# Optimization experiments

Measured on AMD Instinct MI355X. Metric: run time of the kernel, lower is better.

Reference implementation:

```python
import jax, jax.numpy as jnp
import numpy as np

MD = 4  # max_displacement
NEG_SLOPE = 0.1

def _lrelu(x):
    return jnp.where(x >= 0, x, NEG_SLOPE * x)

def _conv3x3(x, w, b):
    # x: [B,C,H,W], w: [O,I,3,3]
    y = jax.lax.conv_general_dilated(x, w, (1, 1), 'SAME',
                                     dimension_numbers=('NCHW', 'OIHW', 'NCHW'))
    return y + b[None, :, None, None]

def _correlation(x_ref, x_nb, md=MD):
    # FlowNet-style correlation, kernel_size=1, stride1=stride2=1, pad=md.
    # out[:, dy*(2md+1)+dx, h, w] = mean_c x_ref[:,c,h,w] * x_nb_pad[:,c,h+dy,w+dx]
    B, C, H, W = x_ref.shape
    xp = jnp.pad(x_nb, ((0, 0), (0, 0), (md, md), (md, md)))
    outs = []
    for dy in range(2 * md + 1):
        for dx in range(2 * md + 1):
            sh = jax.lax.dynamic_slice(xp, (0, 0, dy, dx), (B, C, H, W))
            outs.append(jnp.einsum('bchw,bchw->bhw', x_ref, sh))
    return jnp.stack(outs, axis=1) / C  # [B, (2md+1)^2, H, W]

def _resize2x(x):
    # matches torch F.interpolate(scale_factor=2, mode='bilinear', align_corners=False)
    B, C, H, W = x.shape
    return jax.image.resize(x, (B, C, 2 * H, 2 * W), method='linear')

def setup_inputs() -> dict:
    key = jax.random.key(0)
    ks = jax.random.split(key, 12)
    B, C, H, W = 4, 32, 256, 256
    inner = 32
    corr_dim = (2 * MD + 1) ** 2  # 81
    cin = corr_dim + 32 + 2       # 115
    def wconv(k, o, i):
        return jax.random.normal(k, (o, i, 3, 3), jnp.float32) * 0.05
    return {
        'x_ref': jax.random.normal(ks[0], (B, C, H, W), jnp.float32),
        'x_neighbor': jax.random.normal(ks[1], (B, C, H, W), jnp.float32),
        'base_flow': jax.random.normal(ks[2], (B, 1, 2, H // 2, W // 2), jnp.float32),
        'base_feature': jax.random.normal(ks[3], (B, 32, H // 2, W // 2), jnp.float32),
        'w0': wconv(ks[4], inner, cin), 'b0': jnp.zeros((inner,), jnp.float32),
        'w1': wconv(ks[5], inner, inner), 'b1': jnp.zeros((inner,), jnp.float32),
        'w2': wconv(ks[6], inner, inner), 'b2': jnp.zeros((inner,), jnp.float32),
        'wf': wconv(ks[7], 3, inner), 'bf': jnp.zeros((3,), jnp.float32),
    }

def reference(x_ref, x_neighbor, base_flow, base_feature,
              w0, b0, w1, b1, w2, b2, wf, bf):
    corr = _lrelu(_correlation(x_ref, x_neighbor))           # [B,81,H,W]
    input_feats = _resize2x(base_feature)                    # [B,32,H,W]
    B, nf, two, h2, w2_ = base_flow.shape
    bflow = _resize2x(base_flow.reshape(B, nf * two, h2, w2_)) * 2.0  # [B,2,H,W]
    inp = jnp.concatenate([corr, input_feats, bflow], axis=1)  # [B,115,H,W]
    h = _lrelu(_conv3x3(inp, w0, b0))
    # BasicBlock
    t = _conv3x3(_lrelu(_conv3x3(h, w1, b1)), w2, b2) + h
    feats = _lrelu(t)                                        # [B,32,H,W]
    fm = _conv3x3(feats, wf, bf)                             # [B,3,H,W]
    flow_x, flow_y, mask = jnp.split(fm, 3, axis=1)
    flows = jnp.stack([flow_x, flow_y], axis=1)              # [B,2,1,H,W]
    mask = jax.nn.sigmoid(mask)
    return flows, mask, feats
```

## Files before the change

kernel.cpp:

```cpp
#include <hip/hip_runtime.h>

typedef unsigned short u16;
typedef unsigned int u32;
typedef __bf16 bf16x8 __attribute__((ext_vector_type(8)));
typedef float f32x4 __attribute__((ext_vector_type(4)));

#define HP 258
#define E_WT0 0
#define E_WT1 37120
#define E_WT2 46592
#define E_WTF 56064
#define C_CH      4260096ull
#define OFF_INPT  131072ull
#define S_INPT    17040384ull
#define OFF_HT    68292608ull
#define S_H       4260096ull
#define OFF_T1    85332992ull
#define OFF_FEA   102373376ull
#define OFF_XREFT 119413760ull
#define S_XREF    4194304ull
#define OFF_XNBT  136190976ull
#define S_XNB     4595712ull
#define WS_NEED   154573824ull
#define SE_INPT 8520192u
#define SE_H    2130048u
#define SE_XREF 2097152u
#define SE_XNB  2297856u

__device__ __forceinline__ float bf2f(u16 u){ u32 x = ((u32)u) << 16; return __builtin_bit_cast(float, x); }
__device__ __forceinline__ u16 f2bf(float f){
  u32 x = __builtin_bit_cast(u32, f);
  return (u16)((x + 0x7fffu + ((x >> 16) & 1u)) >> 16);
}
__device__ __forceinline__ u32 pack2(float a, float b){ return (u32)f2bf(a) | ((u32)f2bf(b) << 16); }
__device__ __forceinline__ float lrelu(float x){ return x >= 0.f ? x : 0.1f * x; }

__global__ void k_sent(float* __restrict__ out, float val){
  if (threadIdx.x == 0 && blockIdx.x == 0) out[0] = val;
}

__global__ __launch_bounds__(256) void k_halo(char* __restrict__ ws){
  int idx = blockIdx.x * 256 + threadIdx.x;
  const int bio = blockIdx.y;
  if (idx >= 258 * 258) return;
  int y = idx / 258;
  int x = idx - y * 258;
  if (y != 0 && y != 257 && x != 0 && x != 257) return;
  uint4 z = make_uint4(0u, 0u, 0u, 0u);
  size_t pix = (size_t)idx;
  #pragma unroll
  for (int s = 0; s < 4; s++){
    uint4* p0 = (uint4*)(ws + OFF_INPT + (size_t)bio * S_INPT + (size_t)s * C_CH + pix * 64);
    #pragma unroll
    for (int k = 0; k < 4; k++) p0[k] = z;
  }
  uint4* p1 = (uint4*)(ws + OFF_HT  + (size_t)bio * S_H + pix * 64);
  uint4* p2 = (uint4*)(ws + OFF_T1  + (size_t)bio * S_H + pix * 64);
  uint4* p3 = (uint4*)(ws + OFF_FEA + (size_t)bio * S_H + pix * 64);
  #pragma unroll
  for (int k = 0; k < 4; k++){ p1[k] = z; p2[k] = z; p3[k] = z; }
}

__global__ __launch_bounds__(256) void k_wprep(const float* __restrict__ w0, const float* __restrict__ w1,
    const float* __restrict__ w2, const float* __restrict__ wf, u16* __restrict__ wse){
  for (int idx = blockIdx.x * 256 + threadIdx.x; idx < 60800; idx += 64 * 256){
    float v = 0.f;
    if (idx < 37120){
      int co = idx / 1160, kk = idx % 1160;
      if (kk < 1152){
        int tap = kk >> 7, c = kk & 127;
        if (c < 115){
          int oc = (c < 34) ? (81 + c) : (c - 34);
          v = w0[(co * 115 + oc) * 9 + tap];
        }
      }
    } else if (idx < 46592){
      int r = idx - 37120; int co = r / 296, kk = r % 296;
      if (kk < 288){ int tap = kk >> 5, c = kk & 31; v = w1[(co * 32 + c) * 9 + tap]; }
    } else if (idx < 56064){
      int r = idx - 46592; int co = r / 296, kk = r % 296;
      if (kk < 288){ int tap = kk >> 5, c = kk & 31; v = w2[(co * 32 + c) * 9 + tap]; }
    } else {
      int r = idx - 56064; int co = r / 296, kk = r % 296;
      if (kk < 288 && co < 3){ int tap = kk >> 5, c = kk & 31; v = wf[(co * 32 + c) * 9 + tap]; }
    }
    wse[idx] = f2bf(v);
  }
}

__global__ __launch_bounds__(64) void k_xpose(const float* __restrict__ xref,
    const float* __restrict__ xnb, u16* __restrict__ xrefT0, u16* __restrict__ xnbT0){
  const int l = threadIdx.x;
  const int bxx = blockIdx.x;
  const int bio = blockIdx.y;
  const int cq = l & 3, c0 = cq * 8;
  float v[8];
  u32 p[4];
  if (bxx < 4096){
    const int row = bxx >> 4;
    const int px = ((bxx & 15) << 4) + (l >> 2);
    const float* src = xref + ((size_t)(bio * 32 + c0)) * 65536 + (size_t)row * 256 + px;
    #pragma unroll
    for (int k = 0; k < 8; k++) v[k] = src[(size_t)k * 65536];
    #pragma unroll
    for (int j = 0; j < 4; j++) p[j] = pack2(v[2 * j], v[2 * j + 1]);
    *(uint4*)(xrefT0 + (size_t)bio * SE_XREF + ((size_t)row * 256 + px) * 32 + c0) = *(uint4*)p;
  } else {
    const int i = bxx - 4096;
    const int hp = i / 17, pg = i - hp * 17;
    const int pt = pg * 16 + (l >> 2);
    const int ih = hp - 4, px = pt - 4;
    u16* dst = xnbT0 + (size_t)bio * SE_XNB + ((size_t)hp * 272 + pt) * 32 + c0;
    if (ih >= 0 && ih <= 255 && px >= 0 && px <= 255){
      const float* src = xnb + ((size_t)(bio * 32 + c0)) * 65536 + (size_t)ih * 256 + px;
      #pragma unroll
      for (int k = 0; k < 8; k++) v[k] = src[(size_t)k * 65536];
      #pragma unroll
      for (int j = 0; j < 4; j++) p[j] = pack2(v[2 * j], v[2 * j + 1]);
      *(uint4*)dst = *(uint4*)p;
    } else {
      uint4 z = make_uint4(0u, 0u, 0u, 0u);
      *(uint4*)dst = z;
    }
  }
}

__global__ __launch_bounds__(256) void k_up(const float* __restrict__ bflow,
    const float* __restrict__ bfeat, char* __restrict__ ws){
  const int w = threadIdx.x;
  const int bx = blockIdx.x;
  const int bio = blockIdx.y;
  const int h = (bx & 7) * 32 + (bx >> 3);
  int y0 = (h >> 1) - 1 + (h & 1);
  const float fy = (h & 1) ? 0.25f : 0.75f;
  const int y0o = (y0 < 0 ? 0 : y0) * 128;
  const int y1o = ((y0 + 1) > 127 ? 127 : (y0 + 1)) * 128;
  int x0 = (w >> 1) - 1 + (w & 1);
  const float fx = (w & 1) ? 0.25f : 0.75f;
  const int x0c = x0 < 0 ? 0 : x0;
  const int x1c = (x0 + 1) > 127 ? 127 : (x0 + 1);

  char* pxb = ws + OFF_INPT + (size_t)bio * S_INPT + ((size_t)(h + 1) * 258 + (w + 1)) * 64;

  u32 pk[16];
  #pragma unroll
  for (int d = 0; d < 16; d++){
    float vv[2];
    #pragma unroll
    for (int e = 0; e < 2; e++){
      const float* pl = bfeat + ((size_t)(bio * 32 + 2 * d + e)) * 16384;
      float v00 = pl[y0o + x0c], v01 = pl[y0o + x1c];
      float v10 = pl[y1o + x0c], v11 = pl[y1o + x1c];
      float r0 = v00 + fx * (v01 - v00);
      float r1 = v10 + fx * (v11 - v10);
      vv[e] = r0 + fy * (r1 - r0);
    }
    pk[d] = pack2(vv[0], vv[1]);
  }
  uint4* dst0 = (uint4*)pxb;
  #pragma unroll
  for (int q = 0; q < 4; q++) dst0[q] = ((uint4*)pk)[q];

  float fv[2];
  #pragma unroll
  for (int e = 0; e < 2; e++){
    const float* pl = bflow + ((size_t)(bio * 2 + e)) * 16384;
    float v00 = pl[y0o + x0c], v01 = pl[y0o + x1c];
    float v10 = pl[y1o + x0c], v11 = pl[y1o + x1c];
    float r0 = v00 + fx * (v01 - v00);
    float r1 = v10 + fx * (v11 - v10);
    fv[e] = (r0 + fy * (r1 - r0)) * 2.f;
  }
  *(u32*)(pxb + C_CH) = pack2(fv[0], fv[1]);

  *(u16*)(pxb + 3 * C_CH + 38) = 0;
  #pragma unroll
  for (int k2 = 0; k2 < 6; k2++) *(u32*)(pxb + 3 * C_CH + 40 + 4 * k2) = 0;
}

__global__ __launch_bounds__(256) void k_corr_mfma(const u16* __restrict__ xrefT0,
    const u16* __restrict__ xnbT0, char* __restrict__ ws){
  const int tid = threadIdx.x;
  const int wv = tid >> 6, l = tid & 63;
  const int bx = blockIdx.x;
  const int bio = blockIdx.y;
  const u16* xrefT = xrefT0 + (size_t)bio * SE_XREF;
  const u16* xnbT  = xnbT0  + (size_t)bio * SE_XNB;
  const int r = bx & 255, sub = bx >> 8;
  const int h = (r & 7) * 32 + (r >> 3);
  const int w0 = (sub * 4 + wv) * 16;
  const int m16 = l & 15, g = l >> 4;

  uint4 ua = *(const uint4*)(xrefT + ((size_t)h * 256 + w0 + m16) * 32 + g * 8);
  bf16x8 av = __builtin_bit_cast(bf16x8, ua);

  size_t bOff = ((size_t)h * 272 + w0 + m16) * 32 + g * 8;
  char* ob = ws + OFF_INPT + (size_t)bio * S_INPT
             + ((size_t)(h + 1) * 258 + (w0 + 1) + g * 4) * 64;
  const f32x4 z = {0.f, 0.f, 0.f, 0.f};
  #pragma unroll
  for (int dy = 0; dy < 9; dy++){
    uint4 ub0 = *(const uint4*)(xnbT + bOff);
    uint4 ub1 = *(const uint4*)(xnbT + bOff + 512);
    bOff += 8704;
    f32x4 d0 = __builtin_amdgcn_mfma_f32_16x16x32_bf16(av, __builtin_bit_cast(bf16x8, ub0), z, 0, 0, 0);
    f32x4 d1 = __builtin_amdgcn_mfma_f32_16x16x32_bf16(av, __builtin_bit_cast(bf16x8, ub1), z, 0, 0, 0);
    #pragma unroll
    for (int j = 0; j < 4; j++){
      int dxa = m16 - g * 4 - j;
      int dxb = dxa + 16;
      bool va = (unsigned)dxa <= 8u;
      bool vb = (unsigned)dxb <= 8u;
      if (va | vb){
        float val = va ? d0[j] : d1[j];
        int dx = va ? dxa : dxb;
        float f = lrelu(val * 0.03125f);
        int c = 34 + dy * 9 + dx;
        *(u16*)(ob + j * 64 + (size_t)(c >> 5) * C_CH + (c & 31) * 2) = f2bf(f);
      }
    }
  }
}

__global__ __launch_bounds__(256) void k_conv0(const u16* __restrict__ inT0, const u16* __restrict__ wt,
    const float* __restrict__ bias, u16* __restrict__ outA0){
  __shared__ __align__(16) u16 inL[12672];
  const int tid = threadIdx.x;
  const int bx = blockIdx.x;
  const int bio = blockIdx.y;
  const u16* inT = inT0 + (size_t)bio * SE_INPT;
  u16* outA = outA0 + (size_t)bio * SE_H;
  const int rq = (bx & 7) * 8 + ((bx >> 3) & 7);
  const int ph = bx >> 6;
  const int row0 = rq * 4, p0 = ph * 64;
  const int wv = tid >> 6, ln = tid & 63, l15 = ln & 15, l4 = ln >> 4;
  f32x4 acc[4][2] = {};

  for (int s = 0; s < 4; s++){
    for (int i = tid; i < 1584; i += 256){
      int rr = i / 264, q = i - rr * 264;
      int pxi = q >> 2, cq = q & 3;
      const u16* src = inT + ((size_t)s * 66564 + (size_t)(row0 + rr) * 258 + (p0 + pxi)) * 32 + cq * 8;
      ((uint4*)inL)[(rr * 66 + pxi) * 4 + cq] = *(const uint4*)src;
    }
    __syncthreads();
    #pragma unroll
    for (int ky = 0; ky < 3; ky++){
      #pragma unroll
      for (int kx = 0; kx < 3; kx++){
        const int tap = ky * 3 + kx;
        bf16x8 bv[2];
        #pragma unroll
        for (int j = 0; j < 2; j++){
          uint4 u = *(const uint4*)(wt + (size_t)(j * 16 + l15) * 1160 + tap * 128 + s * 32 + l4 * 8);
          bv[j] = __builtin_bit_cast(bf16x8, u);
        }
        #pragma unroll
        for (int t = 0; t < 4; t++){
          uint4 uai = *(const uint4*)&inL[((wv + ky) * 66 + t * 16 + l15 + kx) * 32 + l4 * 8];
          bf16x8 av = __builtin_bit_cast(bf16x8, uai);
          #pragma unroll
          for (int j = 0; j < 2; j++)
            acc[t][j] = __builtin_amdgcn_mfma_f32_16x16x32_bf16(av, bv[j], acc[t][j], 0, 0, 0);
        }
      }
    }
    __syncthreads();
  }
  const int row = row0 + wv;
  #pragma unroll
  for (int t = 0; t < 4; t++){
    const int pxb = p0 + t * 16 + l4 * 4;
    #pragma unroll
    for (int j = 0; j < 2; j++){
      const int co = j * 16 + l15;
      const float bs = bias[co];
      #pragma unroll
      for (int r = 0; r < 4; r++){
        const int px = pxb + r;
        float v = lrelu(acc[t][j][r] + bs);
        outA[(size_t)((row + 1) * HP + px + 1) * 32 + co] = f2bf(v);
      }
    }
  }
}

template<int NT, int MODE>
__global__ __launch_bounds__(256) void k_conv32(const u16* __restrict__ inT0, const u16* __restrict__ wt,
    const float* __restrict__ bias, u16* __restrict__ outH0, float* __restrict__ outF,
    const u16* __restrict__ resid0){
  __shared__ __align__(16) u16 inL[12672];
  const int tid = threadIdx.x;
  const int bx = blockIdx.x;
  const int bio = blockIdx.y;
  const u16* inT = inT0 + (size_t)bio * SE_H;
  const int rq = (bx & 7) * 8 + ((bx >> 3) & 7);
  const int ph = bx >> 6;
  const int row0 = rq * 4, p0 = ph * 64;
  const int wv = tid >> 6, ln = tid & 63, l15 = ln & 15, l4 = ln >> 4;

  for (int i = tid; i < 1584; i += 256){
    int rr = i / 264, q = i - rr * 264;
    int pxi = q >> 2, cq = q & 3;
    const u16* src = inT + ((size_t)(row0 + rr) * 258 + (p0 + pxi)) * 32 + cq * 8;
    ((uint4*)inL)[(rr * 66 + pxi) * 4 + cq] = *(const uint4*)src;
  }
  __syncthreads();

  f32x4 acc[4][NT] = {};
  #pragma unroll
  for (int ky = 0; ky < 3; ky++){
    #pragma unroll
    for (int kx = 0; kx < 3; kx++){
      const int tap = ky * 3 + kx;
      bf16x8 bv[NT];
      #pragma unroll
      for (int j = 0; j < NT; j++){
        uint4 u = *(const uint4*)(wt + (size_t)(j * 16 + l15) * 296 + tap * 32 + l4 * 8);
        bv[j] = __builtin_bit_cast(bf16x8, u);
      }
      #pragma unroll
      for (int t = 0; t < 4; t++){
        uint4 uai = *(const uint4*)&inL[((wv + ky) * 66 + t * 16 + l15 + kx) * 32 + l4 * 8];
        bf16x8 av = __builtin_bit_cast(bf16x8, uai);
        #pragma unroll
        for (int j = 0; j < NT; j++)
          acc[t][j] = __builtin_amdgcn_mfma_f32_16x16x32_bf16(av, bv[j], acc[t][j], 0, 0, 0);
      }
    }
  }
  const int row = row0 + wv;
  #pragma unroll
  for (int t = 0; t < 4; t++){
    const int pxb = p0 + t * 16 + l4 * 4;
    #pragma unroll
    for (int j = 0; j < NT; j++){
      const int co = j * 16 + l15;
      float bs;
      if constexpr (MODE == 2) bs = (co < 3) ? bias[co] : 0.f;
      else bs = bias[co];
      #pragma unroll
      for (int r = 0; r < 4; r++){
        const int px = pxb + r;
        float v = acc[t][j][r] + bs;
        if constexpr (MODE == 0){
          v = lrelu(v);
          outH0[(size_t)bio * SE_H + (size_t)((row + 1) * HP + px + 1) * 32 + co] = f2bf(v);
        } else if constexpr (MODE == 1){
          float hres = bf2f(resid0[(size_t)bio * SE_H + (size_t)((row + 1) * HP + px + 1) * 32 + co]);
          v = lrelu(v + hres);
          outH0[(size_t)bio * SE_H + (size_t)((row + 1) * HP + px + 1) * 32 + co] = f2bf(v);
          outF[786432 + ((size_t)(bio * 32 + co)) * 65536 + (size_t)row * 256 + px] = v;
        } else {
          if (co < 2)
            outF[((size_t)(bio * 2 + co)) * 65536 + (size_t)row * 256 + px] = v;
          else if (co == 2){
            float s = 1.f / (1.f + __expf(-v));
            outF[524288 + (size_t)bio * 65536 + (size_t)row * 256 + px] = s;
          }
        }
      }
    }
  }
}

extern "C" void kernel_launch(void* const* d_in, const int* in_sizes, int n_in,
                              void* d_out, int out_size, void* d_ws, size_t ws_size,
                              hipStream_t stream){
  float* out = (float*)d_out;

  static const int exp_sizes[12] = {8388608, 8388608, 131072, 2097152,
                                    33120, 32, 9216, 32, 9216, 32, 864, 3};
  float sent = 0.f;
  if (n_in != 12) sent = 1.0e6f;
  else if (out_size != 9175040) sent = 2.0e6f;
  else {
    for (int i = 0; i < 12; i++)
      if (in_sizes[i] != exp_sizes[i]){ sent = 3.0e6f * (1.0f + 0.01f * i); break; }
    if (sent == 0.f && ws_size < WS_NEED)
      sent = 16.0f * (float)(ws_size >> 20);
  }
  if (sent != 0.f){
    hipLaunchKernelGGL(k_sent, dim3(1), dim3(64), 0, stream, out, sent);
    return;
  }

  const float* xref  = (const float*)d_in[0];
  const float* xnb   = (const float*)d_in[1];
  const float* bflow = (const float*)d_in[2];
  const float* bfeat = (const float*)d_in[3];
  const float* w0 = (const float*)d_in[4];
  const float* b0 = (const float*)d_in[5];
  const float* w1 = (const float*)d_in[6];
  const float* b1 = (const float*)d_in[7];
  const float* w2 = (const float*)d_in[8];
  const float* b2 = (const float*)d_in[9];
  const float* wf = (const float*)d_in[10];
  const float* bf = (const float*)d_in[11];
  char* ws = (char*)d_ws;
  u16* wse   = (u16*)d_ws;
  u16* inpT  = (u16*)(ws + OFF_INPT);
  u16* hT    = (u16*)(ws + OFF_HT);
  u16* t1T   = (u16*)(ws + OFF_T1);
  u16* feaT  = (u16*)(ws + OFF_FEA);
  u16* xrefT = (u16*)(ws + OFF_XREFT);
  u16* xnbT  = (u16*)(ws + OFF_XNBT);

  hipLaunchKernelGGL(k_halo, dim3(261, 4), dim3(256), 0, stream, ws);
  hipLaunchKernelGGL(k_wprep, dim3(64), dim3(256), 0, stream, w0, w1, w2, wf, wse);
  hipLaunchKernelGGL(k_xpose, dim3(8584, 4), dim3(64), 0, stream, xref, xnb, xrefT, xnbT);
  hipLaunchKernelGGL(k_up, dim3(256, 4), dim3(256), 0, stream, bflow, bfeat, ws);
  hipLaunchKernelGGL(k_corr_mfma, dim3(1024, 4), dim3(256), 0, stream, xrefT, xnbT, ws);
  hipLaunchKernelGGL(k_conv0, dim3(256, 4), dim3(256), 0, stream, inpT, wse + E_WT0, b0, hT);
  hipLaunchKernelGGL((k_conv32<2, 0>), dim3(256, 4), dim3(256), 0, stream,
                     hT, wse + E_WT1, b1, t1T, (float*)nullptr, (const u16*)nullptr);
  hipLaunchKernelGGL((k_conv32<2, 1>), dim3(256, 4), dim3(256), 0, stream,
                     t1T, wse + E_WT2, b2, feaT, out, hT);
  hipLaunchKernelGGL((k_conv32<1, 2>), dim3(256, 4), dim3(256), 0, stream,
                     feaT, wse + E_WTF, bf, (u16*)nullptr, out, (const u16*)nullptr);
}
```

Measured before the change: 279.4 us.

## Merge prep kernels into one launch and XOR-swizzle conv LDS tiles

Four preprocessing kernels (halo zeroing, weight conversion, input transpose, upsample) are merged into a single k_prep launch that branches on block index, with the transpose using 256-thread blocks covering four waves each. This removes three launches and their gaps and lets the independent prep work run concurrently. The conv kernels also XOR-swizzle the channel-quad index in shared memory by pixel, to reduce LDS bank conflicts on the 16-byte MFMA operand reads. The merged kernel trades some branch divergence and less specialised blocks for fewer launches.

```diff
diff --git a/kernel.cpp b/kernel.cpp
--- a/kernel.cpp
+++ b/kernel.cpp
@@ -39,143 +39,141 @@
   if (threadIdx.x == 0 && blockIdx.x == 0) out[0] = val;
 }
 
-__global__ __launch_bounds__(256) void k_halo(char* __restrict__ ws){
-  int idx = blockIdx.x * 256 + threadIdx.x;
-  const int bio = blockIdx.y;
-  if (idx >= 258 * 258) return;
-  int y = idx / 258;
-  int x = idx - y * 258;
-  if (y != 0 && y != 257 && x != 0 && x != 257) return;
-  uint4 z = make_uint4(0u, 0u, 0u, 0u);
-  size_t pix = (size_t)idx;
-  #pragma unroll
-  for (int s = 0; s < 4; s++){
-    uint4* p0 = (uint4*)(ws + OFF_INPT + (size_t)bio * S_INPT + (size_t)s * C_CH + pix * 64);
-    #pragma unroll
-    for (int k = 0; k < 4; k++) p0[k] = z;
-  }
-  uint4* p1 = (uint4*)(ws + OFF_HT  + (size_t)bio * S_H + pix * 64);
-  uint4* p2 = (uint4*)(ws + OFF_T1  + (size_t)bio * S_H + pix * 64);
-  uint4* p3 = (uint4*)(ws + OFF_FEA + (size_t)bio * S_H + pix * 64);
-  #pragma unroll
-  for (int k = 0; k < 4; k++){ p1[k] = z; p2[k] = z; p3[k] = z; }
-}
-
-__global__ __launch_bounds__(256) void k_wprep(const float* __restrict__ w0, const float* __restrict__ w1,
-    const float* __restrict__ w2, const float* __restrict__ wf, u16* __restrict__ wse){
-  for (int idx = blockIdx.x * 256 + threadIdx.x; idx < 60800; idx += 64 * 256){
-    float v = 0.f;
-    if (idx < 37120){
-      int co = idx / 1160, kk = idx % 1160;
-      if (kk < 1152){
-        int tap = kk >> 7, c = kk & 127;
-        if (c < 115){
-          int oc = (c < 34) ? (81 + c) : (c - 34);
-          v = w0[(co * 115 + oc) * 9 + tap];
-        }
-      }
-    } else if (idx < 46592){
-      int r = idx - 37120; int co = r / 296, kk = r % 296;
-      if (kk < 288){ int tap = kk >> 5, c = kk & 31; v = w1[(co * 32 + c) * 9 + tap]; }
-    } else if (idx < 56064){
-      int r = idx - 46592; int co = r / 296, kk = r % 296;
-      if (kk < 288){ int tap = kk >> 5, c = kk & 31; v = w2[(co * 32 + c) * 9 + tap]; }
-    } else {
-      int r = idx - 56064; int co = r / 296, kk = r % 296;
-      if (kk < 288 && co < 3){ int tap = kk >> 5, c = kk & 31; v = wf[(co * 32 + c) * 9 + tap]; }
-    }
-    wse[idx] = f2bf(v);
-  }
-}
-
-__global__ __launch_bounds__(64) void k_xpose(const float* __restrict__ xref,
-    const float* __restrict__ xnb, u16* __restrict__ xrefT0, u16* __restrict__ xnbT0){
-  const int l = threadIdx.x;
+__global__ __launch_bounds__(256) void k_prep(const float* __restrict__ xref,
+    const float* __restrict__ xnb, const float* __restrict__ bflow,
+    const float* __restrict__ bfeat, const float* __restrict__ w0,
+    const float* __restrict__ w1, const float* __restrict__ w2,
+    const float* __restrict__ wf, char* __restrict__ ws){
+  const int tid = threadIdx.x;
   const int bxx = blockIdx.x;
   const int bio = blockIdx.y;
-  const int cq = l & 3, c0 = cq * 8;
-  float v[8];
-  u32 p[4];
-  if (bxx < 4096){
-    const int row = bxx >> 4;
-    const int px = ((bxx & 15) << 4) + (l >> 2);
-    const float* src = xref + ((size_t)(bio * 32 + c0)) * 65536 + (size_t)row * 256 + px;
-    #pragma unroll
-    for (int k = 0; k < 8; k++) v[k] = src[(size_t)k * 65536];
-    #pragma unroll
-    for (int j = 0; j < 4; j++) p[j] = pack2(v[2 * j], v[2 * j + 1]);
-    *(uint4*)(xrefT0 + (size_t)bio * SE_XREF + ((size_t)row * 256 + px) * 32 + c0) = *(uint4*)p;
-  } else {
-    const int i = bxx - 4096;
-    const int hp = i / 17, pg = i - hp * 17;
-    const int pt = pg * 16 + (l >> 2);
-    const int ih = hp - 4, px = pt - 4;
-    u16* dst = xnbT0 + (size_t)bio * SE_XNB + ((size_t)hp * 272 + pt) * 32 + c0;
-    if (ih >= 0 && ih <= 255 && px >= 0 && px <= 255){
-      const float* src = xnb + ((size_t)(bio * 32 + c0)) * 65536 + (size_t)ih * 256 + px;
+
+  if (bxx < 2146){
+    u16* xrefT0 = (u16*)(ws + OFF_XREFT);
+    u16* xnbT0  = (u16*)(ws + OFF_XNBT);
+    const int wvi = bxx * 4 + (tid >> 6);
+    const int l = tid & 63;
+    const int cq = l & 3, c0 = cq * 8;
+    float v[8];
+    u32 p[4];
+    if (wvi < 4096){
+      const int row = wvi >> 4;
+      const int px = ((wvi & 15) << 4) + (l >> 2);
+      const float* src = xref + ((size_t)(bio * 32 + c0)) * 65536 + (size_t)row * 256 + px;
       #pragma unroll
       for (int k = 0; k < 8; k++) v[k] = src[(size_t)k * 65536];
       #pragma unroll
       for (int j = 0; j < 4; j++) p[j] = pack2(v[2 * j], v[2 * j + 1]);
-      *(uint4*)dst = *(uint4*)p;
+      *(uint4*)(xrefT0 + (size_t)bio * SE_XREF + ((size_t)row * 256 + px) * 32 + c0) = *(uint4*)p;
     } else {
-      uint4 z = make_uint4(0u, 0u, 0u, 0u);
-      *(uint4*)dst = z;
-    }
-  }
-}
-
-__global__ __launch_bounds__(256) void k_up(const float* __restrict__ bflow,
-    const float* __restrict__ bfeat, char* __restrict__ ws){
-  const int w = threadIdx.x;
-  const int bx = blockIdx.x;
-  const int bio = blockIdx.y;
-  const int h = (bx & 7) * 32 + (bx >> 3);
-  int y0 = (h >> 1) - 1 + (h & 1);
-  const float fy = (h & 1) ? 0.25f : 0.75f;
-  const int y0o = (y0 < 0 ? 0 : y0) * 128;
-  const int y1o = ((y0 + 1) > 127 ? 127 : (y0 + 1)) * 128;
-  int x0 = (w >> 1) - 1 + (w & 1);
-  const float fx = (w & 1) ? 0.25f : 0.75f;
-  const int x0c = x0 < 0 ? 0 : x0;
-  const int x1c = (x0 + 1) > 127 ? 127 : (x0 + 1);
-
-  char* pxb = ws + OFF_INPT + (size_t)bio * S_INPT + ((size_t)(h + 1) * 258 + (w + 1)) * 64;
-
-  u32 pk[16];
-  #pragma unroll
-  for (int d = 0; d < 16; d++){
-    float vv[2];
+      const int i = wvi - 4096;
+      const int hp = i / 17, pg = i - hp * 17;
+      const int pt = pg * 16 + (l >> 2);
+      const int ih = hp - 4, px = pt - 4;
+      u16* dst = xnbT0 + (size_t)bio * SE_XNB + ((size_t)hp * 272 + pt) * 32 + c0;
+      if (ih >= 0 && ih <= 255 && px >= 0 && px <= 255){
+        const float* src = xnb + ((size_t)(bio * 32 + c0)) * 65536 + (size_t)ih * 256 + px;
+        #pragma unroll
+        for (int k = 0; k < 8; k++) v[k] = src[(size_t)k * 65536];
+        #pragma unroll
+        for (int j = 0; j < 4; j++) p[j] = pack2(v[2 * j], v[2 * j + 1]);
+        *(uint4*)dst = *(uint4*)p;
+      } else {
+        uint4 z = make_uint4(0u, 0u, 0u, 0u);
+        *(uint4*)dst = z;
+      }
+    }
+  } else if (bxx < 2402){
+    const int ubx = bxx - 2146;
+    const int w = tid;
+    const int h = (ubx & 7) * 32 + (ubx >> 3);
+    int y0 = (h >> 1) - 1 + (h & 1);
+    const float fy = (h & 1) ? 0.25f : 0.75f;
+    const int y0o = (y0 < 0 ? 0 : y0) * 128;
+    const int y1o = ((y0 + 1) > 127 ? 127 : (y0 + 1)) * 128;
+    int x0 = (w >> 1) - 1 + (w & 1);
+    const float fx = (w & 1) ? 0.25f : 0.75f;
+    const int x0c = x0 < 0 ? 0 : x0;
+    const int x1c = (x0 + 1) > 127 ? 127 : (x0 + 1);
+    char* pxb = ws + OFF_INPT + (size_t)bio * S_INPT + ((size_t)(h + 1) * 258 + (w + 1)) * 64;
+    u32 pk[16];
+    #pragma unroll
+    for (int d = 0; d < 16; d++){
+      float vv[2];
+      #pragma unroll
+      for (int e = 0; e < 2; e++){
+        const float* pl = bfeat + ((size_t)(bio * 32 + 2 * d + e)) * 16384;
+        float v00 = pl[y0o + x0c], v01 = pl[y0o + x1c];
+        float v10 = pl[y1o + x0c], v11 = pl[y1o + x1c];
+        float r0 = v00 + fx * (v01 - v00);
+        float r1 = v10 + fx * (v11 - v10);
+        vv[e] = r0 + fy * (r1 - r0);
+      }
+      pk[d] = pack2(vv[0], vv[1]);
+    }
+    uint4* dst0 = (uint4*)pxb;
+    #pragma unroll
+    for (int q = 0; q < 4; q++) dst0[q] = ((uint4*)pk)[q];
+    float fv[2];
     #pragma unroll
     for (int e = 0; e < 2; e++){
-      const float* pl = bfeat + ((size_t)(bio * 32 + 2 * d + e)) * 16384;
+      const float* pl = bflow + ((size_t)(bio * 2 + e)) * 16384;
       float v00 = pl[y0o + x0c], v01 = pl[y0o + x1c];
       float v10 = pl[y1o + x0c], v11 = pl[y1o + x1c];
       float r0 = v00 + fx * (v01 - v00);
       float r1 = v10 + fx * (v11 - v10);
-      vv[e] = r0 + fy * (r1 - r0);
-    }
-    pk[d] = pack2(vv[0], vv[1]);
-  }
-  uint4* dst0 = (uint4*)pxb;
-  #pragma unroll
-  for (int q = 0; q < 4; q++) dst0[q] = ((uint4*)pk)[q];
-
-  float fv[2];
-  #pragma unroll
-  for (int e = 0; e < 2; e++){
-    const float* pl = bflow + ((size_t)(bio * 2 + e)) * 16384;
-    float v00 = pl[y0o + x0c], v01 = pl[y0o + x1c];
-    float v10 = pl[y1o + x0c], v11 = pl[y1o + x1c];
-    float r0 = v00 + fx * (v01 - v00);
-    float r1 = v10 + fx * (v11 - v10);
-    fv[e] = (r0 + fy * (r1 - r0)) * 2.f;
-  }
-  *(u32*)(pxb + C_CH) = pack2(fv[0], fv[1]);
-
-  *(u16*)(pxb + 3 * C_CH + 38) = 0;
-  #pragma unroll
-  for (int k2 = 0; k2 < 6; k2++) *(u32*)(pxb + 3 * C_CH + 40 + 4 * k2) = 0;
+      fv[e] = (r0 + fy * (r1 - r0)) * 2.f;
+    }
+    *(u32*)(pxb + C_CH) = pack2(fv[0], fv[1]);
+    *(u16*)(pxb + 3 * C_CH + 38) = 0;
+    #pragma unroll
+    for (int k2 = 0; k2 < 6; k2++) *(u32*)(pxb + 3 * C_CH + 40 + 4 * k2) = 0;
+  } else if (bxx < 2663){
+    int idx = (bxx - 2402) * 256 + tid;
+    if (idx >= 258 * 258) return;
+    int y = idx / 258;
+    int x = idx - y * 258;
+    if (y != 0 && y != 257 && x != 0 && x != 257) return;
+    uint4 z = make_uint4(0u, 0u, 0u, 0u);
+    size_t pix = (size_t)idx;
+    #pragma unroll
+    for (int s = 0; s < 4; s++){
+      uint4* q0 = (uint4*)(ws + OFF_INPT + (size_t)bio * S_INPT + (size_t)s * C_CH + pix * 64);
+      #pragma unroll
+      for (int k = 0; k < 4; k++) q0[k] = z;
+    }
+    uint4* q1 = (uint4*)(ws + OFF_HT  + (size_t)bio * S_H + pix * 64);
+    uint4* q2 = (uint4*)(ws + OFF_T1  + (size_t)bio * S_H + pix * 64);
+    uint4* q3 = (uint4*)(ws + OFF_FEA + (size_t)bio * S_H + pix * 64);
+    #pragma unroll
+    for (int k = 0; k < 4; k++){ q1[k] = z; q2[k] = z; q3[k] = z; }
+  } else {
+    if (bio != 0) return;
+    u16* wse = (u16*)ws;
+    for (int idx = (bxx - 2663) * 256 + tid; idx < 60800; idx += 4096){
+      float v = 0.f;
+      if (idx < 37120){
+        int co = idx / 1160, kk = idx % 1160;
+        if (kk < 1152){
+          int tap = kk >> 7, c = kk & 127;
+          if (c < 115){
+            int oc = (c < 34) ? (81 + c) : (c - 34);
+            v = w0[(co * 115 + oc) * 9 + tap];
+          }
+        }
+      } else if (idx < 46592){
+        int r = idx - 37120; int co = r / 296, kk = r % 296;
+        if (kk < 288){ int tap = kk >> 5, c = kk & 31; v = w1[(co * 32 + c) * 9 + tap]; }
+      } else if (idx < 56064){
+        int r = idx - 46592; int co = r / 296, kk = r % 296;
+        if (kk < 288){ int tap = kk >> 5, c = kk & 31; v = w2[(co * 32 + c) * 9 + tap]; }
+      } else {
+        int r = idx - 56064; int co = r / 296, kk = r % 296;
+        if (kk < 288 && co < 3){ int tap = kk >> 5, c = kk & 31; v = wf[(co * 32 + c) * 9 + tap]; }
+      }
+      wse[idx] = f2bf(v);
+    }
+  }
 }
 
 __global__ __launch_bounds__(256) void k_corr_mfma(const u16* __restrict__ xrefT0,
@@ -241,7 +239,7 @@
       int rr = i / 264, q = i - rr * 264;
       int pxi = q >> 2, cq = q & 3;
       const u16* src = inT + ((size_t)s * 66564 + (size_t)(row0 + rr) * 258 + (p0 + pxi)) * 32 + cq * 8;
-      ((uint4*)inL)[(rr * 66 + pxi) * 4 + cq] = *(const uint4*)src;
+      ((uint4*)inL)[(rr * 66 + pxi) * 4 + (cq ^ ((pxi >> 1) & 3))] = *(const uint4*)src;
     }
     __syncthreads();
     #pragma unroll
@@ -257,7 +255,8 @@
         }
         #pragma unroll
         for (int t = 0; t < 4; t++){
-          uint4 uai = *(const uint4*)&inL[((wv + ky) * 66 + t * 16 + l15 + kx) * 32 + l4 * 8];
+          const int pxL = t * 16 + l15 + kx;
+          uint4 uai = ((const uint4*)inL)[((wv + ky) * 66 + pxL) * 4 + (l4 ^ ((pxL >> 1) & 3))];
           bf16x8 av = __builtin_bit_cast(bf16x8, uai);
           #pragma unroll
           for (int j = 0; j < 2; j++)
@@ -303,7 +302,7 @@
     int rr = i / 264, q = i - rr * 264;
     int pxi = q >> 2, cq = q & 3;
     const u16* src = inT + ((size_t)(row0 + rr) * 258 + (p0 + pxi)) * 32 + cq * 8;
-    ((uint4*)inL)[(rr * 66 + pxi) * 4 + cq] = *(const uint4*)src;
+    ((uint4*)inL)[(rr * 66 + pxi) * 4 + (cq ^ ((pxi >> 1) & 3))] = *(const uint4*)src;
   }
   __syncthreads();
 
@@ -321,7 +320,8 @@
       }
       #pragma unroll
       for (int t = 0; t < 4; t++){
-        uint4 uai = *(const uint4*)&inL[((wv + ky) * 66 + t * 16 + l15 + kx) * 32 + l4 * 8];
+        const int pxL = t * 16 + l15 + kx;
+        uint4 uai = ((const uint4*)inL)[((wv + ky) * 66 + pxL) * 4 + (l4 ^ ((pxL >> 1) & 3))];
         bf16x8 av = __builtin_bit_cast(bf16x8, uai);
         #pragma unroll
         for (int j = 0; j < NT; j++)
@@ -406,10 +406,8 @@
   u16* xrefT = (u16*)(ws + OFF_XREFT);
   u16* xnbT  = (u16*)(ws + OFF_XNBT);
 
-  hipLaunchKernelGGL(k_halo, dim3(261, 4), dim3(256), 0, stream, ws);
-  hipLaunchKernelGGL(k_wprep, dim3(64), dim3(256), 0, stream, w0, w1, w2, wf, wse);
-  hipLaunchKernelGGL(k_xpose, dim3(8584, 4), dim3(64), 0, stream, xref, xnb, xrefT, xnbT);
-  hipLaunchKernelGGL(k_up, dim3(256, 4), dim3(256), 0, stream, bflow, bfeat, ws);
+  hipLaunchKernelGGL(k_prep, dim3(2679, 4), dim3(256), 0, stream,
+                     xref, xnb, bflow, bfeat, w0, w1, w2, wf, ws);
   hipLaunchKernelGGL(k_corr_mfma, dim3(1024, 4), dim3(256), 0, stream, xrefT, xnbT, ws);
   hipLaunchKernelGGL(k_conv0, dim3(256, 4), dim3(256), 0, stream, inpT, wse + E_WT0, b0, hT);
   hipLaunchKernelGGL((k_conv32<2, 0>), dim3(256, 4), dim3(256), 0, stream,
```

After: 282.3 us. About the same (+1.0%).
